# Performance work log

Measured on AMD Instinct MI355X. Metric: run time of the kernel, lower is better.

Reference implementation:

```python
import jax, jax.numpy as jnp
import numpy as np

NHEAD = 8
ATTN_EPS = 1e-6
LN_EPS = 1e-5


def _layernorm(y, g, b):
    mu = jnp.mean(y, axis=-1, keepdims=True)
    var = jnp.var(y, axis=-1, keepdims=True)
    return (y - mu) * jax.lax.rsqrt(var + LN_EPS) * g + b


def setup_inputs() -> dict:
    key = jax.random.key(0)
    ks = jax.random.split(key, 6)
    B, L, D = 2, 8192, 1024
    s = 1.0 / np.sqrt(D)
    return {
        "x": jax.random.normal(ks[0], (B, L, D), jnp.float32),
        "Wq": jax.random.normal(ks[1], (D, D), jnp.float32) * s,
        "Wm": jax.random.normal(ks[2], (D, D), jnp.float32) * s,
        "W1": jax.random.normal(ks[3], (D, 2 * D), jnp.float32) * s,
        "W2": jax.random.normal(ks[4], (2 * D, D), jnp.float32) * (1.0 / np.sqrt(2 * D)),
        "g1": jnp.ones((D,), jnp.float32),
        "b1": jnp.zeros((D,), jnp.float32),
        "g2": jnp.ones((D,), jnp.float32),
        "b2": jnp.zeros((D,), jnp.float32),
    }


def reference(x, Wq, Wm, W1, W2, g1, b1, g2, b2):
    B, L, D = x.shape
    H = NHEAD
    d = D // H
    # NOTE: original forward uses q_proj for query, key AND value (faithful).
    q = (x @ Wq).reshape(B, L, H, d)  # [B,L,H,d]
    feat = jax.nn.elu(q) + 1.0        # elu feature map, shared by Q and K
    Q = feat
    K = feat
    V = q / L                          # value = value / v_length
    # KV outer-product sum over sequence: [B,H,d,d]
    KV = jnp.einsum('nshd,nshv->nhdv', K, V)
    # normalizer Z: [B,L,H]
    Ksum = K.sum(axis=1)               # [B,H,d]
    Z = 1.0 / (jnp.einsum('nlhd,nhd->nlh', Q, Ksum) + ATTN_EPS)
    msg = jnp.einsum('nlhd,nhdv,nlh->nlhv', Q, KV, Z) * L  # [B,L,H,d]
    msg = msg.reshape(B, L, D) @ Wm    # merge heads
    x = x + _layernorm(msg, g1, b1)
    # NOTE: MLP is applied to `message`, not the updated x (faithful to source).
    mlp = jax.nn.relu(msg @ W1) @ W2
    x = x + _layernorm(mlp, g2, b2)
    return x
```

## Files before the change

kernel.cpp:

```cpp
#include <hip/hip_runtime.h>
#include <hip/hip_bf16.h>
#include <stdint.h>

#define AS1 __attribute__((address_space(1)))
#define AS3 __attribute__((address_space(3)))

typedef __bf16 bf16x8 __attribute__((ext_vector_type(8)));
typedef __bf16 bf16x2 __attribute__((ext_vector_type(2)));
typedef float  f32x4  __attribute__((ext_vector_type(4)));

static constexpr int kL   = 8192;
static constexpr int kD   = 1024;
static constexpr int kM   = 2 * kL;
static constexpr int kNCH = 32;

__device__ __forceinline__ void async_cp16(__bf16* lds, const __bf16* g) {
    __builtin_amdgcn_global_load_lds((AS1 uint32_t*)g, (AS3 uint32_t*)lds, 16, 0, 0);
}

__device__ __forceinline__ float elu1f(float x) {
    return x > 0.0f ? x + 1.0f : __expf(x);
}

template <int M0>
__device__ __forceinline__ void mfma16(f32x4 (&acc)[8][4], const bf16x8 (&af)[4],
                                       const bf16x8 (&bq)[4]) {
#pragma unroll
    for (int i = 0; i < 4; ++i)
#pragma unroll
        for (int n = 0; n < 4; ++n)
            acc[M0 + i][n] = __builtin_amdgcn_mfma_f32_16x16x32_bf16(af[i], bq[n], acc[M0 + i][n], 0, 0, 0);
}

template <int EPI>
__global__ __launch_bounds__(512, 2) void gemm256(const __bf16* __restrict__ A,
                                                  const __bf16* __restrict__ Bt,
                                                  __bf16* __restrict__ C,
                                                  int M, int N, int K) {
    __shared__ __bf16 As[32768];
    __shared__ __bf16 Bs[32768];
    const int tid  = threadIdx.x;
    const int w    = tid >> 6;
    const int l    = tid & 63;
    const int quad = l >> 4;
    const int l16  = l & 15;
    const int wm   = w >> 2;
    const int wn   = w & 3;
    const int row0 = blockIdx.x * 256;
    const int col0 = blockIdx.y * 256;

    const int srow = l >> 2;
    const int sc   = ((l & 3) - (srow >> 1)) & 3;
    const __bf16* Ag0 = A  + (size_t)(row0 + w * 32 + srow) * K + sc * 8;
    const __bf16* Bg0 = Bt + (size_t)(col0 + w * 32 + srow) * K + sc * 8;
    const size_t r16K = (size_t)16 * K;
    const int NT = K >> 6;

    const int fpos = ((quad + (l16 >> 1)) & 3) * 8;
    const int arow = wm * 4096 + l16 * 32 + fpos;
    const int brow = wn * 2048 + l16 * 32 + fpos;

    f32x4 acc[8][4] = {};

    auto stage_h = [&](int ts, int hh) {
        if (ts >= NT) return;
        const int off = (ts & 1) * 16384 + (hh >> 1) * 8192 + w * 1024;
        const int ko  = ts * 64 + (hh >> 1) * 32;
        if ((hh & 1) == 0) {
            async_cp16(&As[off], Ag0 + ko);
            async_cp16(&As[off + 512], Ag0 + ko + r16K);
        } else {
            async_cp16(&Bs[off], Bg0 + ko);
            async_cp16(&Bs[off + 512], Bg0 + ko + r16K);
        }
    };

    stage_h(0, 0); stage_h(0, 1); stage_h(0, 2); stage_h(0, 3);
    asm volatile("s_waitcnt vmcnt(4)" ::: "memory");
    stage_h(1, 0); stage_h(1, 1); stage_h(1, 2);
    asm volatile("s_waitcnt vmcnt(6)" ::: "memory");
    __builtin_amdgcn_s_barrier();

    for (int t = 0; t < NT; ++t) {
        const int bo = (t & 1) * 16384;
        bf16x8 af[4], bq[4];

#pragma unroll
        for (int i = 0; i < 4; ++i) af[i] = *(const bf16x8*)&As[bo + arow + i * 512];
#pragma unroll
        for (int n = 0; n < 4; ++n) bq[n] = *(const bf16x8*)&Bs[bo + brow + n * 512];
        stage_h(t + 1, 3);
        __builtin_amdgcn_s_barrier();
        asm volatile("s_waitcnt lgkmcnt(0)" ::: "memory");
        __builtin_amdgcn_sched_barrier(0);
        __builtin_amdgcn_s_setprio(1);
        mfma16<0>(acc, af, bq);
        __builtin_amdgcn_s_setprio(0);
        __builtin_amdgcn_s_barrier();

#pragma unroll
        for (int i = 0; i < 4; ++i) af[i] = *(const bf16x8*)&As[bo + arow + 2048 + i * 512];
        stage_h(t + 2, 0);
        __builtin_amdgcn_s_barrier();
        asm volatile("s_waitcnt lgkmcnt(0)" ::: "memory");
        __builtin_amdgcn_sched_barrier(0);
        __builtin_amdgcn_s_setprio(1);
        mfma16<4>(acc, af, bq);
        __builtin_amdgcn_s_setprio(0);
        __builtin_amdgcn_s_barrier();

#pragma unroll
        for (int i = 0; i < 4; ++i) af[i] = *(const bf16x8*)&As[bo + 8192 + arow + i * 512];
#pragma unroll
        for (int n = 0; n < 4; ++n) bq[n] = *(const bf16x8*)&Bs[bo + 8192 + brow + n * 512];
        stage_h(t + 2, 1);
        __builtin_amdgcn_s_barrier();
        asm volatile("s_waitcnt lgkmcnt(0)" ::: "memory");
        __builtin_amdgcn_sched_barrier(0);
        __builtin_amdgcn_s_setprio(1);
        mfma16<0>(acc, af, bq);
        __builtin_amdgcn_s_setprio(0);
        __builtin_amdgcn_s_barrier();

#pragma unroll
        for (int i = 0; i < 4; ++i) af[i] = *(const bf16x8*)&As[bo + 8192 + arow + 2048 + i * 512];
        stage_h(t + 2, 2);
        __builtin_amdgcn_s_barrier();
        asm volatile("s_waitcnt lgkmcnt(0)" ::: "memory");
        __builtin_amdgcn_sched_barrier(0);
        __builtin_amdgcn_s_setprio(1);
        mfma16<4>(acc, af, bq);
        __builtin_amdgcn_s_setprio(0);
        if (t + 2 < NT)       { asm volatile("s_waitcnt vmcnt(6)" ::: "memory"); }
        else if (t + 2 == NT) { asm volatile("s_waitcnt vmcnt(0)" ::: "memory"); }
        __builtin_amdgcn_s_barrier();
    }

#pragma unroll
    for (int m = 0; m < 8; ++m) {
        const int rowb = row0 + wm * 128 + m * 16 + quad * 4;
#pragma unroll
        for (int n = 0; n < 4; ++n) {
            const int col = col0 + wn * 64 + n * 16 + l16;
#pragma unroll
            for (int r = 0; r < 4; ++r) {
                float v = acc[m][n][r];
                if (EPI == 1) v = v > 0.0f ? v : 0.0f;
                C[(size_t)(rowb + r) * N + col] = (__bf16)v;
            }
        }
    }
    (void)M;
}

__global__ __launch_bounds__(256) void cvt_f2b(const float* __restrict__ in,
                                               __bf16* __restrict__ out) {
    const size_t i = ((size_t)blockIdx.x * 256 + threadIdx.x) * 8;
    f32x4 a = *(const f32x4*)(in + i);
    f32x4 b = *(const f32x4*)(in + i + 4);
    bf16x8 o;
#pragma unroll
    for (int j = 0; j < 4; ++j) { o[j] = (__bf16)a[j]; o[4 + j] = (__bf16)b[j]; }
    *(bf16x8*)(out + i) = o;
}

__global__ __launch_bounds__(256) void transpose_f2b(const float* __restrict__ in,
                                                     __bf16* __restrict__ out,
                                                     int R, int Ccols) {
    __shared__ __bf16 tile[32][33];
    const int bc = blockIdx.x * 32;
    const int br = blockIdx.y * 32;
    const int tx = threadIdx.x & 31;
    const int ty = threadIdx.x >> 5;
#pragma unroll
    for (int i = ty; i < 32; i += 8)
        tile[i][tx] = (__bf16)in[(size_t)(br + i) * Ccols + bc + tx];
    __syncthreads();
#pragma unroll
    for (int i = ty; i < 32; i += 8)
        out[(size_t)(bc + i) * R + br + tx] = tile[tx][i];
}

__global__ __launch_bounds__(256) void transpose_q(__bf16* __restrict__ q_io,
                                                   __bf16* __restrict__ qT,
                                                   __bf16* __restrict__ fT) {
    __shared__ __bf16 qs[64 * 130];
    __shared__ __bf16 fs[64 * 130];
    const int bh = blockIdx.x, b = bh >> 3, h = bh & 7;
    const int s0 = blockIdx.y * 64;
    const int t = threadIdx.x;
    const size_t rowbase = (size_t)b * 8388608 + (size_t)h * 128;

#pragma unroll
    for (int c = 0; c < 4; ++c) {
        const int id = c * 256 + t;
        const int r = id >> 4, col = (id & 15) * 8;
        __bf16* gp = q_io + rowbase + (size_t)(s0 + r) * 1024 + col;
        bf16x8 qv = *(const bf16x8*)gp;
        bf16x8 fv;
#pragma unroll
        for (int j = 0; j < 8; ++j) fv[j] = (__bf16)elu1f((float)qv[j]);
        *(bf16x8*)gp = fv;
        const int lb = r * 130 + col;
#pragma unroll
        for (int p = 0; p < 4; ++p) {
            bf16x2 qp = { qv[2 * p], qv[2 * p + 1] };
            bf16x2 fp_ = { fv[2 * p], fv[2 * p + 1] };
            *(bf16x2*)&qs[lb + 2 * p] = qp;
            *(bf16x2*)&fs[lb + 2 * p] = fp_;
        }
    }
    __syncthreads();

    const size_t ob = (size_t)bh * (128 * 8192) + s0;
#pragma unroll
    for (int c = 0; c < 4; ++c) {
        const int id = c * 256 + t;
        const int dk = id >> 3, sch = id & 7;
        bf16x8 ov, fo;
#pragma unroll
        for (int j = 0; j < 8; ++j) {
            ov[j] = qs[(sch * 8 + j) * 130 + dk];
            fo[j] = fs[(sch * 8 + j) * 130 + dk];
        }
        *(bf16x8*)(qT + ob + (size_t)dk * 8192 + sch * 8) = ov;
        *(bf16x8*)(fT + ob + (size_t)dk * 8192 + sch * 8) = fo;
    }
}

__global__ __launch_bounds__(256) void kv_gemm(const __bf16* __restrict__ fT,
                                               const __bf16* __restrict__ qT,
                                               float* __restrict__ KVpart,
                                               float* __restrict__ Kspart) {
    __shared__ __bf16 As[2][128 * 32];
    __shared__ __bf16 Bs[2][128 * 32];
    const int tid  = threadIdx.x;
    const int wave = tid >> 6, lane = tid & 63;
    const int quad = lane >> 4, l16 = lane & 15;
    const int wm = wave & 1, wn = wave >> 1;
    const int bh = blockIdx.x, ch = blockIdx.y;

    f32x4 acc[4][4] = {};
    float ksacc[4] = {};

    const int srow = lane >> 2;
    const int sk8  = ((lane & 3) - (srow >> 1)) & 3;
    const size_t base = (size_t)bh * (128 * 8192) + ch * 256 + sk8 * 8;
    const __bf16* Ag0 = fT + base + (size_t)(wave * 32 + srow) * 8192;
    const __bf16* Bg0 = qT + base + (size_t)(wave * 32 + srow) * 8192;
    const size_t r16 = (size_t)16 * 8192;
    const int ldsw = wave * 1024;
    const int fp = ((quad + (l16 >> 1)) & 3) * 8;
    const int frow = l16 * 32 + fp;
    const int nk = 8;
    {
        async_cp16(&As[0][ldsw], Ag0);
        async_cp16(&As[0][ldsw + 512], Ag0 + r16);
        async_cp16(&Bs[0][ldsw], Bg0);
        async_cp16(&Bs[0][ldsw + 512], Bg0 + r16);
    }
    for (int k = 0; k < nk; ++k) {
        __syncthreads();
        if (k + 1 < nk) {
            const int nb = (k + 1) & 1;
            const int ko = (k + 1) << 5;
            async_cp16(&As[nb][ldsw], Ag0 + ko);
            async_cp16(&As[nb][ldsw + 512], Ag0 + r16 + ko);
            async_cp16(&Bs[nb][ldsw], Bg0 + ko);
            async_cp16(&Bs[nb][ldsw + 512], Bg0 + r16 + ko);
        }
        const __bf16* Asb = As[k & 1];
        const __bf16* Bsb = Bs[k & 1];
        bf16x8 af[4], bfr[4];
#pragma unroll
        for (int i = 0; i < 4; ++i)
            af[i] = *(const bf16x8*)&Asb[(wm * 4 + i) * 512 + frow];
#pragma unroll
        for (int j = 0; j < 4; ++j)
            bfr[j] = *(const bf16x8*)&Bsb[(wn * 4 + j) * 512 + frow];
        if (wn == 0) {
#pragma unroll
            for (int i = 0; i < 4; ++i)
#pragma unroll
                for (int j = 0; j < 8; ++j) ksacc[i] += (float)af[i][j];
        }
#pragma unroll
        for (int i = 0; i < 4; ++i)
#pragma unroll
            for (int j = 0; j < 4; ++j)
                acc[i][j] = __builtin_amdgcn_mfma_f32_16x16x32_bf16(af[i], bfr[j], acc[i][j], 0, 0, 0);
    }

    float* outp = KVpart + (((size_t)bh * kNCH + ch) << 14);
#pragma unroll
    for (int i = 0; i < 4; ++i) {
        const int rowb = wm * 64 + i * 16 + quad * 4;
#pragma unroll
        for (int j = 0; j < 4; ++j) {
            const int col = wn * 64 + j * 16 + l16;
#pragma unroll
            for (int r = 0; r < 4; ++r)
                outp[(rowb + r) * 128 + col] = acc[i][j][r];
        }
    }
    if (wn == 0) {
#pragma unroll
        for (int i = 0; i < 4; ++i) {
            float v = ksacc[i];
            v += __shfl_xor(v, 16);
            v += __shfl_xor(v, 32);
            if (quad == 0)
                Kspart[((size_t)bh * kNCH + ch) * 128 + wm * 64 + i * 16 + l16] = v;
        }
    }
}

__global__ __launch_bounds__(256) void reduce_kv(const float* __restrict__ KVpart,
                                                 const float* __restrict__ Kspart,
                                                 __bf16* __restrict__ KVbT,
                                                 float* __restrict__ Ksum) {
    const int t = threadIdx.x;
    if (blockIdx.x < 1024) {
        const size_t o = (size_t)blockIdx.x * 256 + t;
        const size_t bh = o >> 14;
        const size_t rem = o & 16383;
        float s = 0.f;
#pragma unroll 4
        for (int ch = 0; ch < kNCH; ++ch)
            s += KVpart[((bh * kNCH + ch) << 14) + rem];
        const int dk = (int)(rem >> 7), dv = (int)(rem & 127);
        KVbT[(bh << 14) + dv * 128 + dk] = (__bf16)s;
    } else {
        const int o = (blockIdx.x - 1024) * 256 + t;
        const int bh = o >> 7;
        const int dk = o & 127;
        float s = 0.f;
#pragma unroll 4
        for (int ch = 0; ch < kNCH; ++ch)
            s += Kspart[(bh * kNCH + ch) * 128 + dk];
        Ksum[o] = s;
    }
}

__global__ __launch_bounds__(256) void z_kernel(const __bf16* __restrict__ featG,
                                                const float* __restrict__ Ksum,
                                                float* __restrict__ Zbuf) {
    __shared__ float Ks[128];
    const int t = threadIdx.x;
    const int id0 = blockIdx.x * 256;
    const int bh = id0 >> 13;
    if (t < 32) *(f32x4*)&Ks[t * 4] = *(const f32x4*)(Ksum + bh * 128 + t * 4);
    __syncthreads();
    const int s = (id0 + t) & 8191;
    const int b = bh >> 3, h = bh & 7;
    const __bf16* row = featG + (size_t)b * 8388608 + (size_t)s * 1024 + h * 128;
    float p = 0.f;
#pragma unroll
    for (int c = 0; c < 16; ++c) {
        bf16x8 v = *(const bf16x8*)(row + c * 8);
#pragma unroll
        for (int j = 0; j < 8; ++j) p += (float)v[j] * Ks[c * 8 + j];
    }
    Zbuf[(size_t)bh * 8192 + s] = 1.0f / (p + 1e-6f);
}

__global__ __launch_bounds__(256) void msg_gemm(const __bf16* __restrict__ featG,
                                                const __bf16* __restrict__ KVbT,
                                                const float* __restrict__ Zbuf,
                                                __bf16* __restrict__ msg) {
    __shared__ __bf16 As[2][128 * 32];
    __shared__ __bf16 Bs[2][128 * 32];
    __shared__ float Zs[128];
    const int tid  = threadIdx.x;
    const int wave = tid >> 6, lane = tid & 63;
    const int quad = lane >> 4, l16 = lane & 15;
    const int wm = wave & 1, wn = wave >> 1;
    const int bh = blockIdx.x, b = bh >> 3, h = bh & 7;
    const int row0 = blockIdx.y * 128;

    if (tid < 32)
        *(f32x4*)&Zs[tid * 4] = *(const f32x4*)(Zbuf + (size_t)bh * 8192 + row0 + tid * 4);

    f32x4 acc[4][4] = {};
    const int srow = lane >> 2;
    const int sk8  = ((lane & 3) - (srow >> 1)) & 3;
    const __bf16* Ag0 = featG + (size_t)b * 8388608 + (size_t)(row0 + wave * 32 + srow) * 1024 + h * 128 + sk8 * 8;
    const __bf16* Bg0 = KVbT + ((size_t)bh << 14) + (wave * 32 + srow) * 128 + sk8 * 8;
    const size_t rA16 = (size_t)16 * 1024;
    const size_t rB16 = (size_t)16 * 128;
    const int ldsw = wave * 1024;
    const int fp = ((quad + (l16 >> 1)) & 3) * 8;
    const int frow = l16 * 32 + fp;
    const int nk = 4;
    {
        async_cp16(&As[0][ldsw], Ag0);
        async_cp16(&As[0][ldsw + 512], Ag0 + rA16);
        async_cp16(&Bs[0][ldsw], Bg0);
        async_cp16(&Bs[0][ldsw + 512], Bg0 + rB16);
    }
    for (int k = 0; k < nk; ++k) {
        __syncthreads();
        if (k + 1 < nk) {
            const int nb = (k + 1) & 1;
            const int ko = (k + 1) << 5;
            async_cp16(&As[nb][ldsw], Ag0 + ko);
            async_cp16(&As[nb][ldsw + 512], Ag0 + rA16 + ko);
            async_cp16(&Bs[nb][ldsw], Bg0 + ko);
            async_cp16(&Bs[nb][ldsw + 512], Bg0 + rB16 + ko);
        }
        const __bf16* Asb = As[k & 1];
        const __bf16* Bsb = Bs[k & 1];
        bf16x8 af[4], bfr[4];
#pragma unroll
        for (int i = 0; i < 4; ++i)
            af[i] = *(const bf16x8*)&Asb[(wm * 4 + i) * 512 + frow];
#pragma unroll
        for (int j = 0; j < 4; ++j)
            bfr[j] = *(const bf16x8*)&Bsb[(wn * 4 + j) * 512 + frow];
#pragma unroll
        for (int i = 0; i < 4; ++i)
#pragma unroll
            for (int j = 0; j < 4; ++j)
                acc[i][j] = __builtin_amdgcn_mfma_f32_16x16x32_bf16(af[i], bfr[j], acc[i][j], 0, 0, 0);
    }

    const size_t obase = (size_t)b * 8388608 + (size_t)h * 128;
#pragma unroll
    for (int i = 0; i < 4; ++i) {
        const int lr0 = wm * 64 + i * 16 + quad * 4;
#pragma unroll
        for (int j = 0; j < 4; ++j) {
            const int col = wn * 64 + j * 16 + l16;
#pragma unroll
            for (int r = 0; r < 4; ++r) {
                const float v = acc[i][j][r] * Zs[lr0 + r];
                msg[obase + (size_t)(row0 + lr0 + r) * 1024 + col] = (__bf16)v;
            }
        }
    }
}

template <int BF16BASE>
__global__ __launch_bounds__(256) void ln_res(const void* __restrict__ basep,
                                              const __bf16* __restrict__ y,
                                              const float* __restrict__ g,
                                              const float* __restrict__ bvec,
                                              float* __restrict__ out) {
    const int wave = threadIdx.x >> 6, lane = threadIdx.x & 63;
    const int row = blockIdx.x * 4 + wave;
    const size_t ro = (size_t)row * kD + lane * 16;
    bf16x8 y0 = *(const bf16x8*)(y + ro);
    bf16x8 y1 = *(const bf16x8*)(y + ro + 8);
    float v[16];
    float s = 0.f, sq = 0.f;
#pragma unroll
    for (int j = 0; j < 8; ++j) { v[j] = (float)y0[j]; v[8 + j] = (float)y1[j]; }
#pragma unroll
    for (int j = 0; j < 16; ++j) { s += v[j]; sq += v[j] * v[j]; }
#pragma unroll
    for (int m = 1; m < 64; m <<= 1) { s += __shfl_xor(s, m); sq += __shfl_xor(sq, m); }
    const float mu = s * (1.0f / 1024.0f);
    float var = sq * (1.0f / 1024.0f) - mu * mu;
    if (var < 0.f) var = 0.f;
    const float rstd = rsqrtf(var + 1e-5f);
    const int go = lane * 16;
    float bs[16];
    if (BF16BASE) {
        bf16x8 b0 = *(const bf16x8*)((const __bf16*)basep + ro);
        bf16x8 b1 = *(const bf16x8*)((const __bf16*)basep + ro + 8);
#pragma unroll
        for (int j = 0; j < 8; ++j) { bs[j] = (float)b0[j]; bs[8 + j] = (float)b1[j]; }
    } else {
#pragma unroll
        for (int j = 0; j < 4; ++j) {
            f32x4 bb = *(const f32x4*)((const float*)basep + ro + j * 4);
#pragma unroll
            for (int r = 0; r < 4; ++r) bs[j * 4 + r] = bb[r];
        }
    }
#pragma unroll
    for (int j = 0; j < 4; ++j) {
        f32x4 gg = *(const f32x4*)(g + go + j * 4);
        f32x4 be = *(const f32x4*)(bvec + go + j * 4);
        f32x4 o;
#pragma unroll
        for (int r = 0; r < 4; ++r)
            o[r] = bs[j * 4 + r] + (v[j * 4 + r] - mu) * rstd * gg[r] + be[r];
        *(f32x4*)(out + ro + j * 4) = o;
    }
}

extern "C" void kernel_launch(void* const* d_in, const int* in_sizes, int n_in,
                              void* d_out, int out_size, void* d_ws, size_t ws_size,
                              hipStream_t stream) {
    const float* x  = (const float*)d_in[0];
    const float* Wq = (const float*)d_in[1];
    const float* Wm = (const float*)d_in[2];
    const float* W1 = (const float*)d_in[3];
    const float* W2 = (const float*)d_in[4];
    const float* g1 = (const float*)d_in[5];
    const float* b1 = (const float*)d_in[6];
    const float* g2 = (const float*)d_in[7];
    const float* b2 = (const float*)d_in[8];
    float* out = (float*)d_out;

    const size_t BLD = (size_t)kM * kD;
    __bf16* q    = (__bf16*)d_ws;
    __bf16* msg  = q + BLD;
    __bf16* hbuf = msg + BLD;
    __bf16* WqT  = hbuf + 2 * BLD;
    __bf16* WmT  = WqT + 1048576;
    __bf16* W1T  = WmT + 1048576;
    __bf16* W2T  = W1T + 2097152;
    __bf16* KVb  = W2T + 2097152;
    float* KVpart = (float*)(KVb + 262144);
    float* Kspart = KVpart + (size_t)kNCH * 16 * 16384;
    float* Ksum   = Kspart + (size_t)16 * kNCH * 128;
    const size_t need = ((char*)(Ksum + 2048)) - (char*)d_ws;
    if (ws_size < need) return;

    __bf16* xb   = hbuf;
    __bf16* qT   = hbuf + BLD;
    __bf16* fT   = msg;
    __bf16* msg2 = q;
    __bf16* mlp  = msg;
    float*  Zbuf = KVpart;

    const dim3 blk(256);
    const dim3 blk5(512);

    cvt_f2b<<<dim3((unsigned)(BLD / 2048)), blk, 0, stream>>>(x, xb);
    transpose_f2b<<<dim3(32, 32), blk, 0, stream>>>(Wq, WqT, kD, kD);
    transpose_f2b<<<dim3(32, 32), blk, 0, stream>>>(Wm, WmT, kD, kD);
    transpose_f2b<<<dim3(64, 32), blk, 0, stream>>>(W1, W1T, kD, 2048);
    transpose_f2b<<<dim3(32, 64), blk, 0, stream>>>(W2, W2T, 2048, kD);

    gemm256<0><<<dim3(kM / 256, kD / 256), blk5, 0, stream>>>(xb, WqT, q, kM, kD, kD);
    transpose_q<<<dim3(16, 128), blk, 0, stream>>>(q, qT, fT);
    kv_gemm<<<dim3(16, kNCH), blk, 0, stream>>>(fT, qT, KVpart, Kspart);
    reduce_kv<<<dim3(1032), blk, 0, stream>>>(KVpart, Kspart, KVb, Ksum);
    z_kernel<<<dim3(512), blk, 0, stream>>>(q, Ksum, Zbuf);
    msg_gemm<<<dim3(16, kL / 128), blk, 0, stream>>>(q, KVb, Zbuf, msg);
    gemm256<0><<<dim3(kM / 256, kD / 256), blk5, 0, stream>>>(msg, WmT, msg2, kM, kD, kD);
    ln_res<1><<<dim3(kM / 4), blk, 0, stream>>>(xb, msg2, g1, b1, out);
    gemm256<1><<<dim3(kM / 256, 2048 / 256), blk5, 0, stream>>>(msg2, W1T, hbuf, kM, 2048, kD);
    gemm256<0><<<dim3(kM / 256, kD / 256), blk5, 0, stream>>>(hbuf, W2T, mlp, kM, kD, 2048);
    ln_res<0><<<dim3(kM / 4), blk, 0, stream>>>(out, mlp, g2, b2, out);
    (void)in_sizes; (void)n_in; (void)out_size;
}
```

Before: 477.6 us.

## Fuse ELU and Q transposes into projection GEMM, fold Z into msg GEMM

The Q-projection GEMM gains an epilogue that applies the elu+1 feature map and writes the transposed q and feature tensors directly, which removes the separate transpose_q kernel. The normalizer Z is now computed inside msg_gemm from the A fragments and Ksum, which removes z_kernel and its buffer. The GEMM pipeline depth is cut from two tiles in flight to one, and the KV chunk count is halved. The goal is fewer launches and less global traffic, at the cost of strided 8-byte transposed stores from the GEMM epilogue and less prefetch overlap in every GEMM.

Result: slower. 495.8 us (+3.8%).

```diff
diff --git a/kernel.cpp b/kernel.cpp
--- a/kernel.cpp
+++ b/kernel.cpp
@@ -6,13 +6,14 @@
 #define AS3 __attribute__((address_space(3)))
 
 typedef __bf16 bf16x8 __attribute__((ext_vector_type(8)));
-typedef __bf16 bf16x2 __attribute__((ext_vector_type(2)));
+typedef __bf16 bf16x4 __attribute__((ext_vector_type(4)));
 typedef float  f32x4  __attribute__((ext_vector_type(4)));
 
 static constexpr int kL   = 8192;
 static constexpr int kD   = 1024;
 static constexpr int kM   = 2 * kL;
-static constexpr int kNCH = 32;
+static constexpr int kNCH = 16;
+static constexpr int kSCH = kL / kNCH;
 
 __device__ __forceinline__ void async_cp16(__bf16* lds, const __bf16* g) {
     __builtin_amdgcn_global_load_lds((AS1 uint32_t*)g, (AS3 uint32_t*)lds, 16, 0, 0);
@@ -36,6 +37,8 @@
 __global__ __launch_bounds__(512, 2) void gemm256(const __bf16* __restrict__ A,
                                                   const __bf16* __restrict__ Bt,
                                                   __bf16* __restrict__ C,
+                                                  __bf16* __restrict__ qTp,
+                                                  __bf16* __restrict__ fTp,
                                                   int M, int N, int K) {
     __shared__ __bf16 As[32768];
     __shared__ __bf16 Bs[32768];
@@ -77,8 +80,6 @@
 
     stage_h(0, 0); stage_h(0, 1); stage_h(0, 2); stage_h(0, 3);
     asm volatile("s_waitcnt vmcnt(4)" ::: "memory");
-    stage_h(1, 0); stage_h(1, 1); stage_h(1, 2);
-    asm volatile("s_waitcnt vmcnt(6)" ::: "memory");
     __builtin_amdgcn_s_barrier();
 
     for (int t = 0; t < NT; ++t) {
@@ -89,7 +90,7 @@
         for (int i = 0; i < 4; ++i) af[i] = *(const bf16x8*)&As[bo + arow + i * 512];
 #pragma unroll
         for (int n = 0; n < 4; ++n) bq[n] = *(const bf16x8*)&Bs[bo + brow + n * 512];
-        stage_h(t + 1, 3);
+        stage_h(t + 1, 0);
         __builtin_amdgcn_s_barrier();
         asm volatile("s_waitcnt lgkmcnt(0)" ::: "memory");
         __builtin_amdgcn_sched_barrier(0);
@@ -100,20 +101,22 @@
 
 #pragma unroll
         for (int i = 0; i < 4; ++i) af[i] = *(const bf16x8*)&As[bo + arow + 2048 + i * 512];
-        stage_h(t + 2, 0);
+        stage_h(t + 1, 1);
         __builtin_amdgcn_s_barrier();
         asm volatile("s_waitcnt lgkmcnt(0)" ::: "memory");
         __builtin_amdgcn_sched_barrier(0);
         __builtin_amdgcn_s_setprio(1);
         mfma16<4>(acc, af, bq);
         __builtin_amdgcn_s_setprio(0);
+        if (t + 1 < NT) { asm volatile("s_waitcnt vmcnt(4)" ::: "memory"); }
+        else            { asm volatile("s_waitcnt vmcnt(0)" ::: "memory"); }
         __builtin_amdgcn_s_barrier();
 
 #pragma unroll
         for (int i = 0; i < 4; ++i) af[i] = *(const bf16x8*)&As[bo + 8192 + arow + i * 512];
 #pragma unroll
         for (int n = 0; n < 4; ++n) bq[n] = *(const bf16x8*)&Bs[bo + 8192 + brow + n * 512];
-        stage_h(t + 2, 1);
+        stage_h(t + 1, 2);
         __builtin_amdgcn_s_barrier();
         asm volatile("s_waitcnt lgkmcnt(0)" ::: "memory");
         __builtin_amdgcn_sched_barrier(0);
@@ -124,29 +127,54 @@
 
 #pragma unroll
         for (int i = 0; i < 4; ++i) af[i] = *(const bf16x8*)&As[bo + 8192 + arow + 2048 + i * 512];
-        stage_h(t + 2, 2);
+        stage_h(t + 1, 3);
         __builtin_amdgcn_s_barrier();
         asm volatile("s_waitcnt lgkmcnt(0)" ::: "memory");
         __builtin_amdgcn_sched_barrier(0);
         __builtin_amdgcn_s_setprio(1);
         mfma16<4>(acc, af, bq);
         __builtin_amdgcn_s_setprio(0);
-        if (t + 2 < NT)       { asm volatile("s_waitcnt vmcnt(6)" ::: "memory"); }
-        else if (t + 2 == NT) { asm volatile("s_waitcnt vmcnt(0)" ::: "memory"); }
-        __builtin_amdgcn_s_barrier();
-    }
-
-#pragma unroll
-    for (int m = 0; m < 8; ++m) {
-        const int rowb = row0 + wm * 128 + m * 16 + quad * 4;
-#pragma unroll
-        for (int n = 0; n < 4; ++n) {
-            const int col = col0 + wn * 64 + n * 16 + l16;
-#pragma unroll
-            for (int r = 0; r < 4; ++r) {
-                float v = acc[m][n][r];
-                if (EPI == 1) v = v > 0.0f ? v : 0.0f;
-                C[(size_t)(rowb + r) * N + col] = (__bf16)v;
+        if (t + 1 < NT) { asm volatile("s_waitcnt vmcnt(4)" ::: "memory"); }
+        __builtin_amdgcn_s_barrier();
+    }
+
+    if (EPI == 2) {
+#pragma unroll
+        for (int m = 0; m < 8; ++m) {
+            const int rowb = row0 + wm * 128 + m * 16 + quad * 4;
+            const int bb   = rowb >> 13;
+            const int s    = rowb & 8191;
+#pragma unroll
+            for (int n = 0; n < 4; ++n) {
+                const int col = col0 + wn * 64 + n * 16 + l16;
+                const int h = col >> 7, dk = col & 127;
+                const size_t tbase = (((size_t)(bb * 8 + h) * 128 + dk) << 13) + s;
+                bf16x4 qv, fv;
+#pragma unroll
+                for (int r = 0; r < 4; ++r) {
+                    const float v = acc[m][n][r];
+                    const float f = elu1f(v);
+                    C[(size_t)(rowb + r) * N + col] = (__bf16)f;
+                    qv[r] = (__bf16)v;
+                    fv[r] = (__bf16)f;
+                }
+                *(bf16x4*)(qTp + tbase) = qv;
+                *(bf16x4*)(fTp + tbase) = fv;
+            }
+        }
+    } else {
+#pragma unroll
+        for (int m = 0; m < 8; ++m) {
+            const int rowb = row0 + wm * 128 + m * 16 + quad * 4;
+#pragma unroll
+            for (int n = 0; n < 4; ++n) {
+                const int col = col0 + wn * 64 + n * 16 + l16;
+#pragma unroll
+                for (int r = 0; r < 4; ++r) {
+                    float v = acc[m][n][r];
+                    if (EPI == 1) v = v > 0.0f ? v : 0.0f;
+                    C[(size_t)(rowb + r) * N + col] = (__bf16)v;
+                }
             }
         }
     }
@@ -179,53 +207,6 @@
 #pragma unroll
     for (int i = ty; i < 32; i += 8)
         out[(size_t)(bc + i) * R + br + tx] = tile[tx][i];
-}
-
-__global__ __launch_bounds__(256) void transpose_q(__bf16* __restrict__ q_io,
-                                                   __bf16* __restrict__ qT,
-                                                   __bf16* __restrict__ fT) {
-    __shared__ __bf16 qs[64 * 130];
-    __shared__ __bf16 fs[64 * 130];
-    const int bh = blockIdx.x, b = bh >> 3, h = bh & 7;
-    const int s0 = blockIdx.y * 64;
-    const int t = threadIdx.x;
-    const size_t rowbase = (size_t)b * 8388608 + (size_t)h * 128;
-
-#pragma unroll
-    for (int c = 0; c < 4; ++c) {
-        const int id = c * 256 + t;
-        const int r = id >> 4, col = (id & 15) * 8;
-        __bf16* gp = q_io + rowbase + (size_t)(s0 + r) * 1024 + col;
-        bf16x8 qv = *(const bf16x8*)gp;
-        bf16x8 fv;
-#pragma unroll
-        for (int j = 0; j < 8; ++j) fv[j] = (__bf16)elu1f((float)qv[j]);
-        *(bf16x8*)gp = fv;
-        const int lb = r * 130 + col;
-#pragma unroll
-        for (int p = 0; p < 4; ++p) {
-            bf16x2 qp = { qv[2 * p], qv[2 * p + 1] };
-            bf16x2 fp_ = { fv[2 * p], fv[2 * p + 1] };
-            *(bf16x2*)&qs[lb + 2 * p] = qp;
-            *(bf16x2*)&fs[lb + 2 * p] = fp_;
-        }
-    }
-    __syncthreads();
-
-    const size_t ob = (size_t)bh * (128 * 8192) + s0;
-#pragma unroll
-    for (int c = 0; c < 4; ++c) {
-        const int id = c * 256 + t;
-        const int dk = id >> 3, sch = id & 7;
-        bf16x8 ov, fo;
-#pragma unroll
-        for (int j = 0; j < 8; ++j) {
-            ov[j] = qs[(sch * 8 + j) * 130 + dk];
-            fo[j] = fs[(sch * 8 + j) * 130 + dk];
-        }
-        *(bf16x8*)(qT + ob + (size_t)dk * 8192 + sch * 8) = ov;
-        *(bf16x8*)(fT + ob + (size_t)dk * 8192 + sch * 8) = fo;
-    }
 }
 
 __global__ __launch_bounds__(256) void kv_gemm(const __bf16* __restrict__ fT,
@@ -245,14 +226,14 @@
 
     const int srow = lane >> 2;
     const int sk8  = ((lane & 3) - (srow >> 1)) & 3;
-    const size_t base = (size_t)bh * (128 * 8192) + ch * 256 + sk8 * 8;
+    const size_t base = (size_t)bh * (128 * 8192) + ch * kSCH + sk8 * 8;
     const __bf16* Ag0 = fT + base + (size_t)(wave * 32 + srow) * 8192;
     const __bf16* Bg0 = qT + base + (size_t)(wave * 32 + srow) * 8192;
     const size_t r16 = (size_t)16 * 8192;
     const int ldsw = wave * 1024;
     const int fp = ((quad + (l16 >> 1)) & 3) * 8;
     const int frow = l16 * 32 + fp;
-    const int nk = 8;
+    const int nk = kSCH / 32;
     {
         async_cp16(&As[0][ldsw], Ag0);
         async_cp16(&As[0][ldsw + 512], Ag0 + r16);
@@ -342,35 +323,14 @@
     }
 }
 
-__global__ __launch_bounds__(256) void z_kernel(const __bf16* __restrict__ featG,
-                                                const float* __restrict__ Ksum,
-                                                float* __restrict__ Zbuf) {
-    __shared__ float Ks[128];
-    const int t = threadIdx.x;
-    const int id0 = blockIdx.x * 256;
-    const int bh = id0 >> 13;
-    if (t < 32) *(f32x4*)&Ks[t * 4] = *(const f32x4*)(Ksum + bh * 128 + t * 4);
-    __syncthreads();
-    const int s = (id0 + t) & 8191;
-    const int b = bh >> 3, h = bh & 7;
-    const __bf16* row = featG + (size_t)b * 8388608 + (size_t)s * 1024 + h * 128;
-    float p = 0.f;
-#pragma unroll
-    for (int c = 0; c < 16; ++c) {
-        bf16x8 v = *(const bf16x8*)(row + c * 8);
-#pragma unroll
-        for (int j = 0; j < 8; ++j) p += (float)v[j] * Ks[c * 8 + j];
-    }
-    Zbuf[(size_t)bh * 8192 + s] = 1.0f / (p + 1e-6f);
-}
-
 __global__ __launch_bounds__(256) void msg_gemm(const __bf16* __restrict__ featG,
                                                 const __bf16* __restrict__ KVbT,
-                                                const float* __restrict__ Zbuf,
+                                                const float* __restrict__ Ks,
                                                 __bf16* __restrict__ msg) {
     __shared__ __bf16 As[2][128 * 32];
     __shared__ __bf16 Bs[2][128 * 32];
-    __shared__ float Zs[128];
+    __shared__ float KsS[128];
+    __shared__ float Zsh[128];
     const int tid  = threadIdx.x;
     const int wave = tid >> 6, lane = tid & 63;
     const int quad = lane >> 4, l16 = lane & 15;
@@ -379,9 +339,10 @@
     const int row0 = blockIdx.y * 128;
 
     if (tid < 32)
-        *(f32x4*)&Zs[tid * 4] = *(const f32x4*)(Zbuf + (size_t)bh * 8192 + row0 + tid * 4);
+        *(f32x4*)&KsS[tid * 4] = *(const f32x4*)(Ks + bh * 128 + tid * 4);
 
     f32x4 acc[4][4] = {};
+    float zacc[4] = {};
     const int srow = lane >> 2;
     const int sk8  = ((lane & 3) - (srow >> 1)) & 3;
     const __bf16* Ag0 = featG + (size_t)b * 8388608 + (size_t)(row0 + wave * 32 + srow) * 1024 + h * 128 + sk8 * 8;
@@ -417,6 +378,18 @@
 #pragma unroll
         for (int j = 0; j < 4; ++j)
             bfr[j] = *(const bf16x8*)&Bsb[(wn * 4 + j) * 512 + frow];
+        {
+            f32x4 k0 = *(const f32x4*)&KsS[k * 32 + quad * 8];
+            f32x4 k1 = *(const f32x4*)&KsS[k * 32 + quad * 8 + 4];
+#pragma unroll
+            for (int i = 0; i < 4; ++i) {
+#pragma unroll
+                for (int j = 0; j < 4; ++j) {
+                    zacc[i] += (float)af[i][j] * k0[j];
+                    zacc[i] += (float)af[i][4 + j] * k1[j];
+                }
+            }
+        }
 #pragma unroll
         for (int i = 0; i < 4; ++i)
 #pragma unroll
@@ -424,6 +397,16 @@
                 acc[i][j] = __builtin_amdgcn_mfma_f32_16x16x32_bf16(af[i], bfr[j], acc[i][j], 0, 0, 0);
     }
 
+#pragma unroll
+    for (int i = 0; i < 4; ++i) {
+        float v = zacc[i];
+        v += __shfl_xor(v, 16);
+        v += __shfl_xor(v, 32);
+        if (wn == 0 && quad == 0)
+            Zsh[wm * 64 + i * 16 + l16] = 1.0f / (v + 1e-6f);
+    }
+    __syncthreads();
+
     const size_t obase = (size_t)b * 8388608 + (size_t)h * 128;
 #pragma unroll
     for (int i = 0; i < 4; ++i) {
@@ -433,7 +416,7 @@
             const int col = wn * 64 + j * 16 + l16;
 #pragma unroll
             for (int r = 0; r < 4; ++r) {
-                const float v = acc[i][j][r] * Zs[lr0 + r];
+                const float v = acc[i][j][r] * Zsh[lr0 + r];
                 msg[obase + (size_t)(row0 + lr0 + r) * 1024 + col] = (__bf16)v;
             }
         }
@@ -522,9 +505,9 @@
     __bf16* xb   = hbuf;
     __bf16* qT   = hbuf + BLD;
     __bf16* fT   = msg;
+    __bf16* featG = q;
     __bf16* msg2 = q;
     __bf16* mlp  = msg;
-    float*  Zbuf = KVpart;
 
     const dim3 blk(256);
     const dim3 blk5(512);
@@ -535,16 +518,14 @@
     transpose_f2b<<<dim3(64, 32), blk, 0, stream>>>(W1, W1T, kD, 2048);
     transpose_f2b<<<dim3(32, 64), blk, 0, stream>>>(W2, W2T, 2048, kD);
 
-    gemm256<0><<<dim3(kM / 256, kD / 256), blk5, 0, stream>>>(xb, WqT, q, kM, kD, kD);
-    transpose_q<<<dim3(16, 128), blk, 0, stream>>>(q, qT, fT);
+    gemm256<2><<<dim3(kM / 256, kD / 256), blk5, 0, stream>>>(xb, WqT, featG, qT, fT, kM, kD, kD);
     kv_gemm<<<dim3(16, kNCH), blk, 0, stream>>>(fT, qT, KVpart, Kspart);
     reduce_kv<<<dim3(1032), blk, 0, stream>>>(KVpart, Kspart, KVb, Ksum);
-    z_kernel<<<dim3(512), blk, 0, stream>>>(q, Ksum, Zbuf);
-    msg_gemm<<<dim3(16, kL / 128), blk, 0, stream>>>(q, KVb, Zbuf, msg);
-    gemm256<0><<<dim3(kM / 256, kD / 256), blk5, 0, stream>>>(msg, WmT, msg2, kM, kD, kD);
+    msg_gemm<<<dim3(16, kL / 128), blk, 0, stream>>>(featG, KVb, Ksum, msg);
+    gemm256<0><<<dim3(kM / 256, kD / 256), blk5, 0, stream>>>(msg, WmT, msg2, nullptr, nullptr, kM, kD, kD);
     ln_res<1><<<dim3(kM / 4), blk, 0, stream>>>(xb, msg2, g1, b1, out);
-    gemm256<1><<<dim3(kM / 256, 2048 / 256), blk5, 0, stream>>>(msg2, W1T, hbuf, kM, 2048, kD);
-    gemm256<0><<<dim3(kM / 256, kD / 256), blk5, 0, stream>>>(hbuf, W2T, mlp, kM, kD, 2048);
+    gemm256<1><<<dim3(kM / 256, 2048 / 256), blk5, 0, stream>>>(msg2, W1T, hbuf, nullptr, nullptr, kM, 2048, kD);
+    gemm256<0><<<dim3(kM / 256, kD / 256), blk5, 0, stream>>>(hbuf, W2T, mlp, nullptr, nullptr, kM, kD, 2048);
     ln_res<0><<<dim3(kM / 4), blk, 0, stream>>>(out, mlp, g2, b2, out);
     (void)in_sizes; (void)n_in; (void)out_size;
 }
```

## Fuse normalizer Z computation into msg_gemm and halve KV sequence chunks

Applied to the files above, without the earlier changes.

Removes the separate z_kernel pass. msg_gemm now loads Ksum into LDS and accumulates the Q·Ksum dot product from the A fragments it already holds for the MFMA. It reduces that dot product across lanes with shuffles and writes 1/(z+eps) to shared memory before the epilogue. This avoids a second full read of the feature tensor and one kernel launch. Separately, kv_gemm now uses 16 sequence chunks of 512 instead of 32 of 256, halving the partials that reduce_kv must sum at the cost of fewer blocks and longer per-block loops.

Result: no change. 468.7 us (-1.9%).

```diff
diff --git a/kernel.cpp b/kernel.cpp
--- a/kernel.cpp
+++ b/kernel.cpp
@@ -12,7 +12,8 @@
 static constexpr int kL   = 8192;
 static constexpr int kD   = 1024;
 static constexpr int kM   = 2 * kL;
-static constexpr int kNCH = 32;
+static constexpr int kNCH = 16;
+static constexpr int kSCH = kL / kNCH;
 
 __device__ __forceinline__ void async_cp16(__bf16* lds, const __bf16* g) {
     __builtin_amdgcn_global_load_lds((AS1 uint32_t*)g, (AS3 uint32_t*)lds, 16, 0, 0);
@@ -245,14 +246,14 @@
 
     const int srow = lane >> 2;
     const int sk8  = ((lane & 3) - (srow >> 1)) & 3;
-    const size_t base = (size_t)bh * (128 * 8192) + ch * 256 + sk8 * 8;
+    const size_t base = (size_t)bh * (128 * 8192) + ch * kSCH + sk8 * 8;
     const __bf16* Ag0 = fT + base + (size_t)(wave * 32 + srow) * 8192;
     const __bf16* Bg0 = qT + base + (size_t)(wave * 32 + srow) * 8192;
     const size_t r16 = (size_t)16 * 8192;
     const int ldsw = wave * 1024;
     const int fp = ((quad + (l16 >> 1)) & 3) * 8;
     const int frow = l16 * 32 + fp;
-    const int nk = 8;
+    const int nk = kSCH / 32;
     {
         async_cp16(&As[0][ldsw], Ag0);
         async_cp16(&As[0][ldsw + 512], Ag0 + r16);
@@ -342,35 +343,14 @@
     }
 }
 
-__global__ __launch_bounds__(256) void z_kernel(const __bf16* __restrict__ featG,
-                                                const float* __restrict__ Ksum,
-                                                float* __restrict__ Zbuf) {
-    __shared__ float Ks[128];
-    const int t = threadIdx.x;
-    const int id0 = blockIdx.x * 256;
-    const int bh = id0 >> 13;
-    if (t < 32) *(f32x4*)&Ks[t * 4] = *(const f32x4*)(Ksum + bh * 128 + t * 4);
-    __syncthreads();
-    const int s = (id0 + t) & 8191;
-    const int b = bh >> 3, h = bh & 7;
-    const __bf16* row = featG + (size_t)b * 8388608 + (size_t)s * 1024 + h * 128;
-    float p = 0.f;
-#pragma unroll
-    for (int c = 0; c < 16; ++c) {
-        bf16x8 v = *(const bf16x8*)(row + c * 8);
-#pragma unroll
-        for (int j = 0; j < 8; ++j) p += (float)v[j] * Ks[c * 8 + j];
-    }
-    Zbuf[(size_t)bh * 8192 + s] = 1.0f / (p + 1e-6f);
-}
-
 __global__ __launch_bounds__(256) void msg_gemm(const __bf16* __restrict__ featG,
                                                 const __bf16* __restrict__ KVbT,
-                                                const float* __restrict__ Zbuf,
+                                                const float* __restrict__ Ks,
                                                 __bf16* __restrict__ msg) {
     __shared__ __bf16 As[2][128 * 32];
     __shared__ __bf16 Bs[2][128 * 32];
-    __shared__ float Zs[128];
+    __shared__ float KsS[128];
+    __shared__ float Zsh[128];
     const int tid  = threadIdx.x;
     const int wave = tid >> 6, lane = tid & 63;
     const int quad = lane >> 4, l16 = lane & 15;
@@ -379,9 +359,10 @@
     const int row0 = blockIdx.y * 128;
 
     if (tid < 32)
-        *(f32x4*)&Zs[tid * 4] = *(const f32x4*)(Zbuf + (size_t)bh * 8192 + row0 + tid * 4);
+        *(f32x4*)&KsS[tid * 4] = *(const f32x4*)(Ks + bh * 128 + tid * 4);
 
     f32x4 acc[4][4] = {};
+    float zacc[4] = {};
     const int srow = lane >> 2;
     const int sk8  = ((lane & 3) - (srow >> 1)) & 3;
     const __bf16* Ag0 = featG + (size_t)b * 8388608 + (size_t)(row0 + wave * 32 + srow) * 1024 + h * 128 + sk8 * 8;
@@ -417,6 +398,18 @@
 #pragma unroll
         for (int j = 0; j < 4; ++j)
             bfr[j] = *(const bf16x8*)&Bsb[(wn * 4 + j) * 512 + frow];
+        {
+            f32x4 k0 = *(const f32x4*)&KsS[k * 32 + quad * 8];
+            f32x4 k1 = *(const f32x4*)&KsS[k * 32 + quad * 8 + 4];
+#pragma unroll
+            for (int i = 0; i < 4; ++i) {
+#pragma unroll
+                for (int j = 0; j < 4; ++j) {
+                    zacc[i] += (float)af[i][j] * k0[j];
+                    zacc[i] += (float)af[i][4 + j] * k1[j];
+                }
+            }
+        }
 #pragma unroll
         for (int i = 0; i < 4; ++i)
 #pragma unroll
@@ -424,6 +417,16 @@
                 acc[i][j] = __builtin_amdgcn_mfma_f32_16x16x32_bf16(af[i], bfr[j], acc[i][j], 0, 0, 0);
     }
 
+#pragma unroll
+    for (int i = 0; i < 4; ++i) {
+        float v = zacc[i];
+        v += __shfl_xor(v, 16);
+        v += __shfl_xor(v, 32);
+        if (wn == 0 && quad == 0)
+            Zsh[wm * 64 + i * 16 + l16] = 1.0f / (v + 1e-6f);
+    }
+    __syncthreads();
+
     const size_t obase = (size_t)b * 8388608 + (size_t)h * 128;
 #pragma unroll
     for (int i = 0; i < 4; ++i) {
@@ -433,7 +436,7 @@
             const int col = wn * 64 + j * 16 + l16;
 #pragma unroll
             for (int r = 0; r < 4; ++r) {
-                const float v = acc[i][j][r] * Zs[lr0 + r];
+                const float v = acc[i][j][r] * Zsh[lr0 + r];
                 msg[obase + (size_t)(row0 + lr0 + r) * 1024 + col] = (__bf16)v;
             }
         }
@@ -522,9 +525,9 @@
     __bf16* xb   = hbuf;
     __bf16* qT   = hbuf + BLD;
     __bf16* fT   = msg;
+    __bf16* featG = q;
     __bf16* msg2 = q;
     __bf16* mlp  = msg;
-    float*  Zbuf = KVpart;
 
     const dim3 blk(256);
     const dim3 blk5(512);
@@ -539,8 +542,7 @@
     transpose_q<<<dim3(16, 128), blk, 0, stream>>>(q, qT, fT);
     kv_gemm<<<dim3(16, kNCH), blk, 0, stream>>>(fT, qT, KVpart, Kspart);
     reduce_kv<<<dim3(1032), blk, 0, stream>>>(KVpart, Kspart, KVb, Ksum);
-    z_kernel<<<dim3(512), blk, 0, stream>>>(q, Ksum, Zbuf);
-    msg_gemm<<<dim3(16, kL / 128), blk, 0, stream>>>(q, KVb, Zbuf, msg);
+    msg_gemm<<<dim3(16, kL / 128), blk, 0, stream>>>(featG, KVb, Ksum, msg);
     gemm256<0><<<dim3(kM / 256, kD / 256), blk5, 0, stream>>>(msg, WmT, msg2, kM, kD, kD);
     ln_res<1><<<dim3(kM / 4), blk, 0, stream>>>(xb, msg2, g1, b1, out);
     gemm256<1><<<dim3(kM / 256, 2048 / 256), blk5, 0, stream>>>(msg2, W1T, hbuf, kM, 2048, kD);
```
